# Kernel tuning notes

Measured on AMD Instinct MI355X. Metric: run time of the kernel, lower is better.

Reference implementation:

```python
import jax, jax.numpy as jnp
from jax import lax
import numpy as np

B, N, NPOINTS, DOWN_NUM, K = 4, 4096, 4096, 1024, 16
EPS = 1e-5


def setup_inputs() -> dict:
    key = jax.random.key(0)
    ks = jax.random.split(key, 8)
    w = lambda k, s: jax.random.normal(k, s, jnp.float32) * 0.05
    return {
        "x": jax.random.normal(ks[0], (B, 3, N), jnp.float32),
        "w_in": w(ks[1], (8, 3)), "b_in": jnp.zeros((8,), jnp.float32),
        "w1": w(ks[2], (32, 16)), "g1w": jnp.ones((32,), jnp.float32), "g1b": jnp.zeros((32,), jnp.float32),
        "w2": w(ks[3], (64, 64)), "g2w": jnp.ones((64,), jnp.float32), "g2b": jnp.zeros((64,), jnp.float32),
        "w3": w(ks[4], (64, 128)), "g3w": jnp.ones((64,), jnp.float32), "g3b": jnp.zeros((64,), jnp.float32),
        "w4": w(ks[5], (128, 128)), "g4w": jnp.ones((128,), jnp.float32), "g4b": jnp.zeros((128,), jnp.float32),
    }


def _knn_idx(coor_k, coor_q, k):
    # coor_*: (B,3,N) -> idx (B,Nq,k) of k nearest points in coor_k for each query
    q = coor_q.transpose(0, 2, 1)  # (B,Nq,3)
    r = coor_k.transpose(0, 2, 1)  # (B,Nk,3)
    d = (jnp.sum(q * q, -1)[:, :, None] + jnp.sum(r * r, -1)[:, None, :]
         - 2.0 * jnp.einsum('bqc,bkc->bqk', q, r))
    _, idx = lax.top_k(-d, k)  # smallest distances
    return idx


def _graph_feature(coor_q, x_q, coor_k, x_k, k):
    # gather k-NN neighbor features and concat (neighbor - center, center)
    idx = _knn_idx(coor_k, coor_q, k)           # (B,Nq,k)
    xk = x_k.transpose(0, 2, 1)                  # (B,Nk,C)
    b, nq, _ = idx.shape
    c = xk.shape[-1]
    feat = jnp.take_along_axis(xk, idx.reshape(b, nq * k)[..., None], axis=1)
    feat = feat.reshape(b, nq, k, c).transpose(0, 3, 1, 2)  # (B,C,Nq,k)
    xq = x_q[:, :, :, None]                      # (B,C,Nq,1)
    return jnp.concatenate([feat - xq, jnp.broadcast_to(xq, feat.shape)], axis=1)


def _fps_idx(xyz, m):
    # furthest point sampling, xyz (B,N,3) -> idx (B,m); starts at point 0
    b, n, _ = xyz.shape
    def body(carry, _):
        dists, farthest = carry
        centroid = jnp.take_along_axis(xyz, farthest[:, None, None], axis=1)  # (B,1,3)
        d = jnp.sum((xyz - centroid) ** 2, axis=-1)
        dists = jnp.minimum(dists, d)
        return (dists, jnp.argmax(dists, axis=-1)), farthest
    init = (jnp.full((b, n), 1e10, xyz.dtype), jnp.zeros((b,), jnp.int32))
    _, idx = lax.scan(body, init, None, length=m)
    return idx.T  # (B,m)


def _fps_downsample(coor, f, m):
    idx = _fps_idx(coor.transpose(0, 2, 1), m)        # (B,m)
    combined = jnp.concatenate([coor, f], axis=1)      # (B,3+C,N)
    new = jnp.take_along_axis(combined, idx[:, None, :], axis=2)
    return new[:, :3], new[:, 3:]


def _group_norm(x, w, b, groups=4):
    bsz, c = x.shape[0], x.shape[1]
    xr = x.reshape(bsz, groups, -1)
    m = xr.mean(-1, keepdims=True)
    v = xr.var(-1, keepdims=True)
    xn = ((xr - m) * lax.rsqrt(v + EPS)).reshape(x.shape)
    shp = (1, c) + (1,) * (x.ndim - 2)
    return xn * w.reshape(shp) + b.reshape(shp)


def _block(f, w, gw, gb):
    # 1x1 conv (no bias) -> GroupNorm(4) -> LeakyReLU(0.2) -> max over neighbors
    h = jnp.einsum('oc,bcnk->bonk', w, f)
    h = jax.nn.leaky_relu(_group_norm(h, gw, gb), negative_slope=0.2)
    return h.max(axis=-1)


def reference(x, w_in, b_in, w1, g1w, g1b, w2, g2w, g2b, w3, g3w, g3b, w4, g4w, g4b):
    coor = x
    f = jnp.einsum('oc,bcn->bon', w_in, x) + b_in[None, :, None]
    inpc_f = f
    f = _graph_feature(coor, f, coor, f, K)
    f = _block(f, w1, g1w, g1b)                      # (B,32,N)
    coor_q, f_q = _fps_downsample(coor, f, NPOINTS // 2)
    f = _graph_feature(coor_q, f_q, coor, f, K)
    f = _block(f, w2, g2w, g2b)                      # (B,64,N/2)
    xyz1, point1 = coor_q, f
    coor = coor_q
    f = _graph_feature(coor, f, coor, f, K)
    f = _block(f, w3, g3w, g3b)                      # (B,64,N/2)
    coor_q, f_q = _fps_downsample(coor, f, DOWN_NUM)
    f = _graph_feature(coor_q, f_q, coor, f, K)
    f = _block(f, w4, g4w, g4b)                      # (B,128,DOWN_NUM)
    coor = coor_q
    return (coor, f, xyz1, point1, inpc_f)
```

## Files before the change

kernel.cpp:

```cpp
#include <hip/hip_runtime.h>
#include <float.h>
#include <math.h>

static constexpr int BATCH = 4;
static constexpr int NPT0  = 4096;

static constexpr size_t OFF_F0T  = 0;
static constexpr size_t OFF_F1T  = 524288;
static constexpr size_t OFF_F2T  = 3670016;
static constexpr size_t OFF_F3T  = 5767168;
static constexpr size_t OFF_CQ1  = 8912896;
static constexpr size_t OFF_CQ2  = 9011200;
static constexpr size_t OFF_H    = 9060352;
static constexpr size_t OFF_IDX1 = 42614784;
static constexpr size_t OFF_IDX2 = 43663360;
static constexpr size_t OFF_IDX3 = 44187648;
static constexpr size_t OFF_IDX4 = 44711936;
static constexpr size_t OFF_FPS1 = 44974080;
static constexpr size_t OFF_FPS2 = 45006848;
static constexpr size_t OFF_WD1  = 45023232;
static constexpr size_t OFF_WD2  = 45024256;
static constexpr size_t OFF_WD3  = 45032448;
static constexpr size_t OFF_WD4  = 45048832;
static constexpr size_t OFF_STAT = 45081600;
static constexpr size_t OFF_PART  = 45099008;
static constexpr size_t OFF_PART2 = OFF_PART;
static constexpr size_t OFF_PART3 = OFF_PART + 8388608;
static constexpr size_t OFF_PART4 = OFF_PART + 12582912;

static constexpr size_t OUT_COOR = 0;
static constexpr size_t OUT_F    = 12288;
static constexpr size_t OUT_XYZ1 = 536576;
static constexpr size_t OUT_PT1  = 561152;
static constexpr size_t OUT_INPC = 1085440;

__device__ __forceinline__ void prep_dev(
    int vb, const float* __restrict__ w1, const float* __restrict__ w2,
    const float* __restrict__ w3, const float* __restrict__ w4,
    float* __restrict__ wd1, float* __restrict__ wd2,
    float* __restrict__ wd3, float* __restrict__ wd4,
    double* __restrict__ stats)
{
  int t = vb * 256 + threadIdx.x;
  if (t < 128) stats[t] = 0.0;
  if (t < 32 * 8)   { int o = t / 8,  c = t % 8;  wd1[t] = w1[o*16  + 8   + c] - w1[o*16  + c]; }
  if (t < 64 * 32)  { int o = t / 32, c = t % 32; wd2[t] = w2[o*64  + 32  + c] - w2[o*64  + c]; }
  if (t < 64 * 64)  { int o = t / 64, c = t % 64; wd3[t] = w3[o*128 + 64  + c] - w3[o*128 + c]; }
  if (t < 128 * 64) { int o = t / 64, c = t % 64; wd4[t] = w4[o*128 + 64  + c] - w4[o*128 + c]; }
}

__device__ __forceinline__ void linear_dev(
    int vb, const float* __restrict__ x, const float* __restrict__ w_in,
    const float* __restrict__ b_in, float* __restrict__ f0t,
    float* __restrict__ out_inpc)
{
  int t = vb * 256 + threadIdx.x;
  int n = t & (NPT0 - 1);
  int b = t >> 12;
  float x0 = x[(size_t)b*3*NPT0 + n];
  float x1 = x[(size_t)b*3*NPT0 + NPT0 + n];
  float x2 = x[(size_t)b*3*NPT0 + 2*NPT0 + n];
#pragma unroll
  for (int o = 0; o < 8; ++o) {
    float v = __fmul_rn(w_in[o*3], x0);
    v = fmaf(w_in[o*3+1], x1, v);
    v = fmaf(w_in[o*3+2], x2, v);
    v = __fadd_rn(v, b_in[o]);
    f0t[(size_t)t * 8 + o] = v;
    out_inpc[((size_t)b*8 + o)*NPT0 + n] = v;
  }
}

__device__ __forceinline__ void knnp_dev(
    int vb, const float* __restrict__ cq, const float* __restrict__ ck,
    unsigned long long* __restrict__ part, int Nq, int Nk, int slices, void* smem)
{
  const int CS = 512;
  int s  = vb % slices;
  int r  = vb / slices;
  int qb = r % (Nq >> 8);
  int b  = r / (Nq >> 8);
  float4* cand = (float4*)smem;
  int t = threadIdx.x;
  const float* ckb = ck + (size_t)b*3*Nk;
  for (int jj = t; jj < CS; jj += 256) {
    int j = s*CS + jj;
    float xx = ckb[j], yy = ckb[Nk + j], zz = ckb[2*Nk + j];
    float sq = __fadd_rn(__fadd_rn(__fmul_rn(xx,xx), __fmul_rn(yy,yy)), __fmul_rn(zz,zz));
    cand[jj] = make_float4(xx, yy, zz, sq);
  }
  __syncthreads();
  int q = qb*256 + t;
  const float* cqb = cq + (size_t)b*3*Nq;
  float qx = cqb[q], qy = cqb[Nq + q], qz = cqb[2*Nq + q];
  float sqq = __fadd_rn(__fadd_rn(__fmul_rn(qx,qx), __fmul_rn(qy,qy)), __fmul_rn(qz,qz));

  unsigned long long bd[16];
#pragma unroll
  for (int sl = 0; sl < 16; ++sl) bd[sl] = ~0ull;
  unsigned long long wk = ~0ull; int ws = 0;

  for (int jj = 0; jj < CS; ++jj) {
    float4 c = cand[jj];
    float dot = __fmul_rn(c.x, qx);
    dot = fmaf(c.y, qy, dot);
    dot = fmaf(c.z, qz, dot);
    float d = __fsub_rn(__fadd_rn(sqq, c.w), __fmul_rn(2.0f, dot));
    unsigned u = __float_as_uint(d);
    u ^= (0x80000000u | (unsigned)((int)u >> 31));
    unsigned long long key = ((unsigned long long)u << 32) | (unsigned)(s*CS + jj);
    if (key < wk) {
      unsigned long long nw = 0; int nws = 0;
#pragma unroll
      for (int sl = 0; sl < 16; ++sl) {
        bool rep = (sl == ws);
        unsigned long long v = rep ? key : bd[sl];
        bd[sl] = v;
        bool g = v > nw;
        nw = g ? v : nw; nws = g ? sl : nws;
      }
      wk = nw; ws = nws;
    }
  }
  unsigned long long* op = part + (((size_t)b*Nq + q)*(size_t)slices + s)*16;
#pragma unroll
  for (int sl = 0; sl < 16; ++sl) op[sl] = bd[sl];
}

__device__ __forceinline__ void merge_dev(
    int vb, const unsigned long long* __restrict__ part, int* __restrict__ idx,
    int slices)
{
  int t = vb * 256 + threadIdx.x;
  const unsigned long long* ip = part + (size_t)t * slices * 16;
  unsigned long long bd[16];
#pragma unroll
  for (int sl = 0; sl < 16; ++sl) bd[sl] = ~0ull;
  unsigned long long wk = ~0ull; int ws = 0;
  int n = slices * 16;
  for (int i = 0; i < n; ++i) {
    unsigned long long key = ip[i];
    if (key < wk) {
      unsigned long long nw = 0; int nws = 0;
#pragma unroll
      for (int sl = 0; sl < 16; ++sl) {
        bool rep = (sl == ws);
        unsigned long long v = rep ? key : bd[sl];
        bd[sl] = v;
        bool g = v > nw;
        nw = g ? v : nw; nws = g ? sl : nws;
      }
      wk = nw; ws = nws;
    }
  }
  int* op = idx + (size_t)t * 16;
#pragma unroll
  for (int sl = 0; sl < 16; ++sl) op[sl] = (int)(bd[sl] & 0xFFFFFFFFull);
}

__global__ __launch_bounds__(256) void k_merge(
    const unsigned long long* __restrict__ part, int* __restrict__ idx, int slices)
{
  merge_dev(blockIdx.x, part, idx, slices);
}

template<int NN, int PPT>
__device__ __forceinline__ void fps_dev(
    int b, const float* __restrict__ coor, int m, int* __restrict__ fidx_all,
    float* __restrict__ ca_all, float* __restrict__ co_all, void* smem)
{
  __builtin_amdgcn_s_setprio(3);
  float* sx = (float*)smem;
  float* sy = sx + NN;
  float* sz = sy + NN;
  unsigned long long* part = (unsigned long long*)(sz + NN);
  int t = threadIdx.x, lane = t & 63, wv = t >> 6;
  const float* cb = coor + (size_t)b*3*NN;
  float px[PPT], py[PPT], pz[PPT], pd[PPT];
  unsigned invj[PPT];
#pragma unroll
  for (int i = 0; i < PPT; ++i) {
    int j = i*256 + t;
    px[i] = cb[j]; py[i] = cb[NN + j]; pz[i] = cb[2*NN + j];
    pd[i] = 1e10f;
    invj[i] = (unsigned)(~j);
    sx[j] = px[i]; sy[j] = py[i]; sz[j] = pz[i];
  }
  __syncthreads();
  float cx = sx[0], cy = sy[0], cz = sz[0];
  int* fidx = fidx_all + b*m;
  float* ca = ca_all + (size_t)b*3*m;
  float* co = co_all + (size_t)b*3*m;
  int cur = 0, par = 0;
  for (int it = 0; it < m; ++it) {
    if (t == 0) {
      fidx[it] = cur;
      ca[it] = cx; ca[m + it] = cy; ca[2*m + it] = cz;
      co[it] = cx; co[m + it] = cy; co[2*m + it] = cz;
    }
    unsigned long long kk[PPT];
#pragma unroll
    for (int i = 0; i < PPT; ++i) {
      float dx = __fsub_rn(px[i], cx);
      float dy = __fsub_rn(py[i], cy);
      float dz = __fsub_rn(pz[i], cz);
      float d = __fadd_rn(__fadd_rn(__fmul_rn(dx,dx), __fmul_rn(dy,dy)), __fmul_rn(dz,dz));
      float nd = fminf(pd[i], d);
      pd[i] = nd;
      kk[i] = ((unsigned long long)__float_as_uint(nd) << 32) | invj[i];
    }
#pragma unroll
    for (int st = PPT/2; st >= 1; st >>= 1)
#pragma unroll
      for (int i = 0; i < st; ++i)
        if (kk[i + st] > kk[i]) kk[i] = kk[i + st];
    unsigned long long bk = kk[0];
#pragma unroll
    for (int mm = 1; mm < 64; mm <<= 1) {
      unsigned long long o = __shfl_xor(bk, mm, 64);
      bk = o > bk ? o : bk;
    }
    if (lane == 0) part[par*4 + wv] = bk;
    __syncthreads();
    ulonglong2 p01 = *(ulonglong2*)&part[par*4 + 0];
    ulonglong2 p23 = *(ulonglong2*)&part[par*4 + 2];
    unsigned long long k0 = p01.x > p01.y ? p01.x : p01.y;
    unsigned long long k2 = p23.x > p23.y ? p23.x : p23.y;
    k0 = k2 > k0 ? k2 : k0;
    cur = (int)(~(unsigned)(k0 & 0xFFFFFFFFull));
    cx = sx[cur]; cy = sy[cur]; cz = sz[cur];
    par ^= 1;
  }
}

template<int C, int COUT, int OC>
__device__ __forceinline__ void passA_dev(
    int vb, const float* __restrict__ xq, const float* __restrict__ xk,
    const int* __restrict__ idx, const float* __restrict__ w,
    const float* __restrict__ wdl, float* __restrict__ h,
    double* __restrict__ stats, int Nq, int Nk,
    const int* __restrict__ qmap, int NqSrc, void* smem)
{
  constexpr int NCH = COUT / OC;
  constexpr int GS  = COUT / 4;
  float* sxq   = (float*)smem;
  float* sbase = sxq + 16*C;
  int qb = Nq >> 4;
  int b = vb / qb, nb = vb % qb;
  int n0 = nb << 4;
  int t = threadIdx.x;
  for (int i = t; i < 16*C; i += 256) {
    int nn = i / C, cc = i % C;
    int qrow = qmap ? qmap[b*Nq + n0 + nn] : (n0 + nn);
    sxq[nn*C + cc] = xq[((size_t)b*NqSrc + qrow)*C + cc];
  }
  __syncthreads();
  for (int i = t; i < 16*COUT; i += 256) {
    int nn = i / COUT, o = i % COUT;
    float acc = 0.f;
#pragma unroll 4
    for (int c = 0; c < C; ++c) acc = fmaf(wdl[o*C + c], sxq[nn*C + c], acc);
    sbase[nn*(COUT+1) + o] = acc;
  }
  __syncthreads();
  int lane = t & 63;
  int n_loc = t >> 4, kk = t & 15;
  int kidx = idx[((size_t)b*Nq + n0 + n_loc)*16 + kk];
  const float* xr = xk + ((size_t)b*Nk + kidx)*C;
  float* hrow = h + (((size_t)b*Nq + n0 + n_loc)*16 + kk)*(size_t)COUT;
#pragma unroll 1
  for (int oc = 0; oc < NCH; ++oc) {
    int o0 = oc * OC;
    float acc[OC];
#pragma unroll
    for (int oi = 0; oi < OC; ++oi) acc[oi] = sbase[n_loc*(COUT+1) + o0 + oi];
#pragma unroll 1
    for (int c4 = 0; c4 < C/4; ++c4) {
      float4 v = *(const float4*)(xr + c4*4);
#pragma unroll
      for (int oi = 0; oi < OC; ++oi) {
        const float* wr = w + (size_t)(o0 + oi)*(2*C) + c4*4;
        acc[oi] = fmaf(wr[0], v.x, acc[oi]);
        acc[oi] = fmaf(wr[1], v.y, acc[oi]);
        acc[oi] = fmaf(wr[2], v.z, acc[oi]);
        acc[oi] = fmaf(wr[3], v.w, acc[oi]);
      }
    }
#pragma unroll
    for (int oi = 0; oi < OC; ++oi) hrow[o0 + oi] = acc[oi];
    double s = 0.0, s2 = 0.0;
#pragma unroll
    for (int oi = 0; oi < OC; ++oi) { double dv = (double)acc[oi]; s += dv; s2 += dv*dv; }
#pragma unroll
    for (int mm = 1; mm < 64; mm <<= 1) {
      s  += __shfl_xor(s,  mm, 64);
      s2 += __shfl_xor(s2, mm, 64);
    }
    if (lane == 0) {
      int g = o0 / GS;
      atomicAdd(&stats[((size_t)b*4 + g)*2],     s);
      atomicAdd(&stats[((size_t)b*4 + g)*2 + 1], s2);
    }
  }
}

template<int C, int COUT, int OC>
__global__ __launch_bounds__(256) void k_passA(
    const float* __restrict__ xq, const float* __restrict__ xk,
    const int* __restrict__ idx, const float* __restrict__ w,
    const float* __restrict__ wdl, float* __restrict__ h,
    double* __restrict__ stats, int Nq, int Nk,
    const int* __restrict__ qmap, int NqSrc)
{
  extern __shared__ char smem[];
  passA_dev<C,COUT,OC>(blockIdx.x, xq, xk, idx, w, wdl, h, stats, Nq, Nk,
                       qmap, NqSrc, smem);
}

__device__ __forceinline__ void passB_dev(
    int vb, const float* __restrict__ h, const double* __restrict__ stats,
    const float* __restrict__ gw, const float* __restrict__ gb,
    float* __restrict__ ft, float* __restrict__ ocn, int Nq, int COUT)
{
  int t = vb * 256 + threadIdx.x;
  int o = t % COUT;
  int r = t / COUT;
  int n = r % Nq;
  int b = r / Nq;
  int GS = COUT / 4, g = o / GS;
  double cnt = (double)GS * (double)Nq * 16.0;
  double su = stats[((size_t)b*4 + g)*2];
  double s2 = stats[((size_t)b*4 + g)*2 + 1];
  double mean = su / cnt;
  double var = s2 / cnt - mean * mean;
  float vf = (float)var; if (vf < 0.f) vf = 0.f;
  float inv = 1.0f / sqrtf(vf + 1e-5f);
  float A = gw[o] * inv;
  float Bb = gb[o] - (float)mean * A;
  const float* hp = h + (((size_t)b*Nq + n)*16)*(size_t)COUT + o;
  float m = -FLT_MAX;
#pragma unroll
  for (int k = 0; k < 16; ++k) {
    float v = hp[(size_t)k*COUT];
    float y = fmaf(v, A, Bb);
    y = (y >= 0.f) ? y : 0.2f*y;
    m = fmaxf(m, y);
  }
  if (ft)  ft[((size_t)b*Nq + n)*COUT + o] = m;
  if (ocn) ocn[((size_t)b*COUT + o)*Nq + n] = m;
}

__global__ __launch_bounds__(256) void k_passB(
    const float* __restrict__ h, const double* __restrict__ stats,
    const float* __restrict__ gw, const float* __restrict__ gb,
    float* __restrict__ ft, float* __restrict__ ocn, int Nq, int COUT)
{
  passB_dev(blockIdx.x, h, stats, gw, gb, ft, ocn, Nq, COUT);
}

__global__ __launch_bounds__(256) void k_megaA(
    const float* __restrict__ x, const float* __restrict__ w_in,
    const float* __restrict__ b_in, float* __restrict__ f0t,
    float* __restrict__ outInpc,
    const float* __restrict__ w1, const float* __restrict__ w2,
    const float* __restrict__ w3, const float* __restrict__ w4,
    float* __restrict__ wd1, float* __restrict__ wd2,
    float* __restrict__ wd3, float* __restrict__ wd4,
    double* __restrict__ stats,
    int* __restrict__ fps1, float* __restrict__ cq1, float* __restrict__ outXyz1,
    unsigned long long* __restrict__ part1)
{
  extern __shared__ char smem[];
  int vb = blockIdx.x;
  if      (vb < 4)   fps_dev<4096,16>(vb, x, 2048, fps1, cq1, outXyz1, smem);
  else if (vb < 36)  prep_dev(vb - 4, w1, w2, w3, w4, wd1, wd2, wd3, wd4, stats);
  else if (vb < 100) linear_dev(vb - 36, x, w_in, b_in, f0t, outInpc);
  else               knnp_dev(vb - 100, x, x, part1, 4096, 4096, 8, smem);
}

__global__ __launch_bounds__(256) void k_megaB(
    const float* __restrict__ cq1, const float* __restrict__ x,
    int* __restrict__ fps2, float* __restrict__ cq2, float* __restrict__ outCoor,
    unsigned long long* __restrict__ part2, unsigned long long* __restrict__ part3,
    const float* __restrict__ f0t, const int* __restrict__ idx1,
    const float* __restrict__ w1, const float* __restrict__ wd1,
    float* __restrict__ h, double* __restrict__ st1)
{
  extern __shared__ char smem[];
  int vb = blockIdx.x;
  if      (vb < 4)           fps_dev<2048,8>(vb, cq1, 1024, fps2, cq2, outCoor, smem);
  else if (vb < 4 + 256)     knnp_dev(vb - 4,   cq1, x,   part2, 2048, 4096, 8, smem);
  else if (vb < 4 + 256+128) knnp_dev(vb - 260, cq1, cq1, part3, 2048, 2048, 4, smem);
  else                       passA_dev<8,32,8>(vb - 388, f0t, f0t, idx1, w1, wd1,
                                               h, st1, 4096, 4096, nullptr, 4096, smem);
}

__global__ __launch_bounds__(256) void k_megaC(
    const float* __restrict__ cq2, const float* __restrict__ cq1,
    unsigned long long* __restrict__ part4,
    const unsigned long long* __restrict__ part2, int* __restrict__ idx2,
    const unsigned long long* __restrict__ part3, int* __restrict__ idx3,
    const float* __restrict__ h, const double* __restrict__ st1,
    const float* __restrict__ g1w, const float* __restrict__ g1b,
    float* __restrict__ f1t)
{
  extern __shared__ char smem[];
  int vb = blockIdx.x;
  if      (vb < 64)  knnp_dev(vb, cq2, cq1, part4, 1024, 2048, 4, smem);
  else if (vb < 96)  merge_dev(vb - 64, part2, idx2, 8);
  else if (vb < 128) merge_dev(vb - 96, part3, idx3, 4);
  else               passB_dev(vb - 128, h, st1, g1w, g1b, f1t, nullptr, 4096, 32);
}

__global__ __launch_bounds__(256) void k_megaD(
    const unsigned long long* __restrict__ part4, int* __restrict__ idx4,
    const float* __restrict__ f1t, const int* __restrict__ idx2,
    const float* __restrict__ w2, const float* __restrict__ wd2,
    float* __restrict__ h, double* __restrict__ st2,
    const int* __restrict__ fps1)
{
  extern __shared__ char smem[];
  int vb = blockIdx.x;
  if (vb < 16) merge_dev(vb, part4, idx4, 4);
  else         passA_dev<32,64,16>(vb - 16, f1t, f1t, idx2, w2, wd2, h, st2,
                                   2048, 4096, fps1, 4096, smem);
}

extern "C" void kernel_launch(void* const* d_in, const int* in_sizes, int n_in,
                              void* d_out, int out_size, void* d_ws, size_t ws_size,
                              hipStream_t stream)
{
  (void)in_sizes; (void)n_in; (void)out_size; (void)ws_size;
  const float* x    = (const float*)d_in[0];
  const float* w_in = (const float*)d_in[1];
  const float* b_in = (const float*)d_in[2];
  const float* w1   = (const float*)d_in[3];
  const float* g1w  = (const float*)d_in[4];
  const float* g1b  = (const float*)d_in[5];
  const float* w2   = (const float*)d_in[6];
  const float* g2w  = (const float*)d_in[7];
  const float* g2b  = (const float*)d_in[8];
  const float* w3   = (const float*)d_in[9];
  const float* g3w  = (const float*)d_in[10];
  const float* g3b  = (const float*)d_in[11];
  const float* w4   = (const float*)d_in[12];
  const float* g4w  = (const float*)d_in[13];
  const float* g4b  = (const float*)d_in[14];
  float* out = (float*)d_out;
  char*  wsb = (char*)d_ws;

  float* f0t  = (float*)(wsb + OFF_F0T);
  float* f1t  = (float*)(wsb + OFF_F1T);
  float* f2t  = (float*)(wsb + OFF_F2T);
  float* f3t  = (float*)(wsb + OFF_F3T);
  float* cq1  = (float*)(wsb + OFF_CQ1);
  float* cq2  = (float*)(wsb + OFF_CQ2);
  float* h    = (float*)(wsb + OFF_H);
  int*   idx1 = (int*)(wsb + OFF_IDX1);
  int*   idx2 = (int*)(wsb + OFF_IDX2);
  int*   idx3 = (int*)(wsb + OFF_IDX3);
  int*   idx4 = (int*)(wsb + OFF_IDX4);
  int*   fps1 = (int*)(wsb + OFF_FPS1);
  int*   fps2 = (int*)(wsb + OFF_FPS2);
  float* wd1  = (float*)(wsb + OFF_WD1);
  float* wd2  = (float*)(wsb + OFF_WD2);
  float* wd3  = (float*)(wsb + OFF_WD3);
  float* wd4  = (float*)(wsb + OFF_WD4);
  double* statAll = (double*)(wsb + OFF_STAT);
  double* st1 = statAll, *st2 = statAll + 32, *st3 = statAll + 64, *st4 = statAll + 96;
  unsigned long long* part1 = (unsigned long long*)(wsb + OFF_PART);
  unsigned long long* part2 = (unsigned long long*)(wsb + OFF_PART2);
  unsigned long long* part3 = (unsigned long long*)(wsb + OFF_PART3);
  unsigned long long* part4 = (unsigned long long*)(wsb + OFF_PART4);

  float* outCoor = out + OUT_COOR;
  float* outF    = out + OUT_F;
  float* outXyz1 = out + OUT_XYZ1;
  float* outPt1  = out + OUT_PT1;
  float* outInpc = out + OUT_INPC;

  k_megaA<<<612, 256, 49216, stream>>>(x, w_in, b_in, f0t, outInpc,
      w1, w2, w3, w4, wd1, wd2, wd3, wd4, statAll, fps1, cq1, outXyz1, part1);
  k_merge<<<64, 256, 0, stream>>>(part1, idx1, 8);

  k_megaB<<<1412, 256, 24640, stream>>>(
      cq1, x, fps2, cq2, outCoor, part2, part3, f0t, idx1, w1, wd1, h, st1);

  k_megaC<<<2176, 256, 8192, stream>>>(
      cq2, cq1, part4, part2, idx2, part3, idx3, h, st1, g1w, g1b, f1t);

  k_megaD<<<528, 256, 6208, stream>>>(part4, idx4, f1t, idx2, w2, wd2, h, st2, fps1);

  k_passB<<<2048, 256, 0, stream>>>(h, st2, g2w, g2b, f2t, outPt1, 2048, 64);
  k_passA<64,64,16><<<512, 256, 8256, stream>>>(f2t, f2t, idx3, w3, wd3, h, st3,
                                                2048, 2048, nullptr, 2048);
  k_passB<<<2048, 256, 0, stream>>>(h, st3, g3w, g3b, f3t, nullptr, 2048, 64);
  k_passA<64,128,16><<<256, 256, 12352, stream>>>(f3t, f3t, idx4, w4, wd4, h, st4,
                                                  1024, 2048, fps2, 2048);
  k_passB<<<2048, 256, 0, stream>>>(h, st4, g4w, g4b, nullptr, outF, 1024, 128);
}
```

Measured before the change: 3.397 ms.

## Precompute packed candidate arrays, widen KNN slices, and use DPP reductions in FPS

Adds a pre-kernel that packs candidate coordinates plus squared norms into float4 arrays in global memory. KNN partial blocks now stream these packed candidates directly instead of staging them in LDS, with 1024-wide slices, which halves the slice count and the work in the later merges. The FPS loop replaces the 64-bit key tree and shuffle reduction with a float argmax followed by a DPP row reduction, and drops the priority boost. Kernels are re-split so FPS shares its launch with fewer co-resident blocks; this adds one extra launch and relies on KNN blocks overlapping the serial FPS.

```diff
diff --git a/kernel.cpp b/kernel.cpp
--- a/kernel.cpp
+++ b/kernel.cpp
@@ -25,14 +25,25 @@
 static constexpr size_t OFF_STAT = 45081600;
 static constexpr size_t OFF_PART  = 45099008;
 static constexpr size_t OFF_PART2 = OFF_PART;
-static constexpr size_t OFF_PART3 = OFF_PART + 8388608;
-static constexpr size_t OFF_PART4 = OFF_PART + 12582912;
+static constexpr size_t OFF_PART3 = OFF_PART + 4194304;
+static constexpr size_t OFF_PART4 = OFF_PART + 6291456;
+static constexpr size_t OFF_CAND0 = 53487616;
+static constexpr size_t OFF_CAND1 = 53749760;
 
 static constexpr size_t OUT_COOR = 0;
 static constexpr size_t OUT_F    = 12288;
 static constexpr size_t OUT_XYZ1 = 536576;
 static constexpr size_t OUT_PT1  = 561152;
 static constexpr size_t OUT_INPC = 1085440;
+
+template<int CTRL>
+__device__ __forceinline__ unsigned long long dpp_max64(unsigned long long k) {
+  unsigned lo = (unsigned)k, hi = (unsigned)(k >> 32);
+  unsigned olo = (unsigned)__builtin_amdgcn_update_dpp((int)lo, (int)lo, CTRL, 0xF, 0xF, false);
+  unsigned ohi = (unsigned)__builtin_amdgcn_update_dpp((int)hi, (int)hi, CTRL, 0xF, 0xF, false);
+  unsigned long long o = ((unsigned long long)ohi << 32) | olo;
+  return o > k ? o : k;
+}
 
 __device__ __forceinline__ void prep_dev(
     int vb, const float* __restrict__ w1, const float* __restrict__ w2,
@@ -71,7 +82,59 @@
   }
 }
 
-__device__ __forceinline__ void knnp_dev(
+template<int CS>
+__device__ __forceinline__ void knnp_pack_dev(
+    int vb, const float* __restrict__ cq, const float4* __restrict__ candPack,
+    unsigned long long* __restrict__ part, int Nq, int Nk)
+{
+  const int slices = Nk / CS;
+  int s  = vb % slices;
+  int r  = vb / slices;
+  int qb = r % (Nq >> 8);
+  int b  = r / (Nq >> 8);
+  int t  = threadIdx.x;
+  int q  = qb*256 + t;
+  const float* cqb = cq + (size_t)b*3*Nq;
+  float qx = cqb[q], qy = cqb[Nq + q], qz = cqb[2*Nq + q];
+  float sqq = __fadd_rn(__fadd_rn(__fmul_rn(qx,qx), __fmul_rn(qy,qy)), __fmul_rn(qz,qz));
+
+  const float4* cp = candPack + (size_t)b*Nk + s*CS;
+  int jbase = s*CS;
+
+  unsigned long long bd[16];
+#pragma unroll
+  for (int sl = 0; sl < 16; ++sl) bd[sl] = ~0ull;
+  unsigned long long wk = ~0ull; int ws = 0;
+
+#pragma unroll 4
+  for (int jj = 0; jj < CS; ++jj) {
+    float4 c = cp[jj];
+    float dot = __fmul_rn(c.x, qx);
+    dot = fmaf(c.y, qy, dot);
+    dot = fmaf(c.z, qz, dot);
+    float d = __fsub_rn(__fadd_rn(sqq, c.w), __fmul_rn(2.0f, dot));
+    unsigned u = __float_as_uint(d);
+    u ^= (0x80000000u | (unsigned)((int)u >> 31));
+    unsigned long long key = ((unsigned long long)u << 32) | (unsigned)(jbase + jj);
+    if (key < wk) {
+      unsigned long long nw = 0; int nws = 0;
+#pragma unroll
+      for (int sl = 0; sl < 16; ++sl) {
+        bool rep = (sl == ws);
+        unsigned long long v = rep ? key : bd[sl];
+        bd[sl] = v;
+        bool g = v > nw;
+        nw = g ? v : nw; nws = g ? sl : nws;
+      }
+      wk = nw; ws = nws;
+    }
+  }
+  unsigned long long* op = part + (((size_t)b*Nq + q)*(size_t)slices + s)*16;
+#pragma unroll
+  for (int sl = 0; sl < 16; ++sl) op[sl] = bd[sl];
+}
+
+__device__ __forceinline__ void knnp_lds_dev(
     int vb, const float* __restrict__ cq, const float* __restrict__ ck,
     unsigned long long* __restrict__ part, int Nq, int Nk, int slices, void* smem)
 {
@@ -158,18 +221,11 @@
   for (int sl = 0; sl < 16; ++sl) op[sl] = (int)(bd[sl] & 0xFFFFFFFFull);
 }
 
-__global__ __launch_bounds__(256) void k_merge(
-    const unsigned long long* __restrict__ part, int* __restrict__ idx, int slices)
-{
-  merge_dev(blockIdx.x, part, idx, slices);
-}
-
 template<int NN, int PPT>
 __device__ __forceinline__ void fps_dev(
     int b, const float* __restrict__ coor, int m, int* __restrict__ fidx_all,
     float* __restrict__ ca_all, float* __restrict__ co_all, void* smem)
 {
-  __builtin_amdgcn_s_setprio(3);
   float* sx = (float*)smem;
   float* sy = sx + NN;
   float* sz = sy + NN;
@@ -177,13 +233,11 @@
   int t = threadIdx.x, lane = t & 63, wv = t >> 6;
   const float* cb = coor + (size_t)b*3*NN;
   float px[PPT], py[PPT], pz[PPT], pd[PPT];
-  unsigned invj[PPT];
 #pragma unroll
   for (int i = 0; i < PPT; ++i) {
     int j = i*256 + t;
     px[i] = cb[j]; py[i] = cb[NN + j]; pz[i] = cb[2*NN + j];
     pd[i] = 1e10f;
-    invj[i] = (unsigned)(~j);
     sx[j] = px[i]; sy[j] = py[i]; sz[j] = pz[i];
   }
   __syncthreads();
@@ -198,7 +252,7 @@
       ca[it] = cx; ca[m + it] = cy; ca[2*m + it] = cz;
       co[it] = cx; co[m + it] = cy; co[2*m + it] = cz;
     }
-    unsigned long long kk[PPT];
+    float bv = -1.0f; int bslot = 0;
 #pragma unroll
     for (int i = 0; i < PPT; ++i) {
       float dx = __fsub_rn(px[i], cx);
@@ -207,25 +261,26 @@
       float d = __fadd_rn(__fadd_rn(__fmul_rn(dx,dx), __fmul_rn(dy,dy)), __fmul_rn(dz,dz));
       float nd = fminf(pd[i], d);
       pd[i] = nd;
-      kk[i] = ((unsigned long long)__float_as_uint(nd) << 32) | invj[i];
-    }
-#pragma unroll
-    for (int st = PPT/2; st >= 1; st >>= 1)
-#pragma unroll
-      for (int i = 0; i < st; ++i)
-        if (kk[i + st] > kk[i]) kk[i] = kk[i + st];
-    unsigned long long bk = kk[0];
-#pragma unroll
-    for (int mm = 1; mm < 64; mm <<= 1) {
-      unsigned long long o = __shfl_xor(bk, mm, 64);
-      bk = o > bk ? o : bk;
-    }
-    if (lane == 0) part[par*4 + wv] = bk;
+      bool g = nd > bv;
+      bv = g ? nd : bv;
+      bslot = g ? i : bslot;
+    }
+    unsigned bij = ~(unsigned)((bslot << 8) | t);
+    unsigned long long k = ((unsigned long long)__float_as_uint(bv) << 32) | bij;
+    k = dpp_max64<0x111>(k);
+    k = dpp_max64<0x112>(k);
+    k = dpp_max64<0x114>(k);
+    k = dpp_max64<0x118>(k);
+    k = dpp_max64<0x142>(k);
+    k = dpp_max64<0x143>(k);
+    unsigned wlo = (unsigned)__builtin_amdgcn_readlane((int)(unsigned)k, 63);
+    unsigned whi = (unsigned)__builtin_amdgcn_readlane((int)(unsigned)(k >> 32), 63);
+    if (lane == 0) part[par*4 + wv] = ((unsigned long long)whi << 32) | wlo;
     __syncthreads();
-    ulonglong2 p01 = *(ulonglong2*)&part[par*4 + 0];
-    ulonglong2 p23 = *(ulonglong2*)&part[par*4 + 2];
-    unsigned long long k0 = p01.x > p01.y ? p01.x : p01.y;
-    unsigned long long k2 = p23.x > p23.y ? p23.x : p23.y;
+    unsigned long long k0 = part[par*4 + 0], k1 = part[par*4 + 1];
+    unsigned long long k2 = part[par*4 + 2], k3 = part[par*4 + 3];
+    k0 = k1 > k0 ? k1 : k0;
+    k2 = k3 > k2 ? k3 : k2;
     k0 = k2 > k0 ? k2 : k0;
     cur = (int)(~(unsigned)(k0 & 0xFFFFFFFFull));
     cx = sx[cur]; cy = sy[cur]; cz = sz[cur];
@@ -358,7 +413,7 @@
   passB_dev(blockIdx.x, h, stats, gw, gb, ft, ocn, Nq, COUT);
 }
 
-__global__ __launch_bounds__(256) void k_megaA(
+__global__ __launch_bounds__(256) void k_pre(
     const float* __restrict__ x, const float* __restrict__ w_in,
     const float* __restrict__ b_in, float* __restrict__ f0t,
     float* __restrict__ outInpc,
@@ -366,20 +421,51 @@
     const float* __restrict__ w3, const float* __restrict__ w4,
     float* __restrict__ wd1, float* __restrict__ wd2,
     float* __restrict__ wd3, float* __restrict__ wd4,
-    double* __restrict__ stats,
-    int* __restrict__ fps1, float* __restrict__ cq1, float* __restrict__ outXyz1,
-    unsigned long long* __restrict__ part1)
+    double* __restrict__ stats, float4* __restrict__ cand0)
+{
+  int vb = blockIdx.x;
+  if (vb < 64) {
+    int g = vb*256 + threadIdx.x;
+    int b = g >> 12, n = g & 4095;
+    const float* xb = x + (size_t)b*3*4096;
+    float xx = xb[n], yy = xb[4096 + n], zz = xb[2*4096 + n];
+    float sq = __fadd_rn(__fadd_rn(__fmul_rn(xx,xx), __fmul_rn(yy,yy)), __fmul_rn(zz,zz));
+    cand0[g] = make_float4(xx, yy, zz, sq);
+  }
+  else if (vb < 96) prep_dev(vb - 64, w1, w2, w3, w4, wd1, wd2, wd3, wd4, stats);
+  else              linear_dev(vb - 96, x, w_in, b_in, f0t, outInpc);
+}
+
+__global__ __launch_bounds__(256, 2) void k_megaA(
+    const float* __restrict__ x, int* __restrict__ fps1,
+    float* __restrict__ cq1, float* __restrict__ outXyz1,
+    const float4* __restrict__ cand0, unsigned long long* __restrict__ part1)
 {
   extern __shared__ char smem[];
   int vb = blockIdx.x;
-  if      (vb < 4)   fps_dev<4096,16>(vb, x, 2048, fps1, cq1, outXyz1, smem);
-  else if (vb < 36)  prep_dev(vb - 4, w1, w2, w3, w4, wd1, wd2, wd3, wd4, stats);
-  else if (vb < 100) linear_dev(vb - 36, x, w_in, b_in, f0t, outInpc);
-  else               knnp_dev(vb - 100, x, x, part1, 4096, 4096, 8, smem);
-}
-
-__global__ __launch_bounds__(256) void k_megaB(
-    const float* __restrict__ cq1, const float* __restrict__ x,
+  if (vb < 4) fps_dev<4096,16>(vb, x, 2048, fps1, cq1, outXyz1, smem);
+  else        knnp_pack_dev<1024>(vb - 4, x, cand0, part1, 4096, 4096);
+}
+
+__global__ __launch_bounds__(256) void k_mergeP(
+    const unsigned long long* __restrict__ part1, int* __restrict__ idx1,
+    const float* __restrict__ cq1, float4* __restrict__ cand1)
+{
+  int vb = blockIdx.x;
+  if (vb < 64) merge_dev(vb, part1, idx1, 4);
+  else {
+    int g = (vb - 64)*256 + threadIdx.x;
+    int b = g >> 11, n = g & 2047;
+    const float* cb = cq1 + (size_t)b*3*2048;
+    float xx = cb[n], yy = cb[2048 + n], zz = cb[2*2048 + n];
+    float sq = __fadd_rn(__fadd_rn(__fmul_rn(xx,xx), __fmul_rn(yy,yy)), __fmul_rn(zz,zz));
+    cand1[g] = make_float4(xx, yy, zz, sq);
+  }
+}
+
+__global__ __launch_bounds__(256, 2) void k_megaB(
+    const float* __restrict__ cq1, const float4* __restrict__ cand0,
+    const float4* __restrict__ cand1,
     int* __restrict__ fps2, float* __restrict__ cq2, float* __restrict__ outCoor,
     unsigned long long* __restrict__ part2, unsigned long long* __restrict__ part3,
     const float* __restrict__ f0t, const int* __restrict__ idx1,
@@ -388,11 +474,11 @@
 {
   extern __shared__ char smem[];
   int vb = blockIdx.x;
-  if      (vb < 4)           fps_dev<2048,8>(vb, cq1, 1024, fps2, cq2, outCoor, smem);
-  else if (vb < 4 + 256)     knnp_dev(vb - 4,   cq1, x,   part2, 2048, 4096, 8, smem);
-  else if (vb < 4 + 256+128) knnp_dev(vb - 260, cq1, cq1, part3, 2048, 2048, 4, smem);
-  else                       passA_dev<8,32,8>(vb - 388, f0t, f0t, idx1, w1, wd1,
-                                               h, st1, 4096, 4096, nullptr, 4096, smem);
+  if      (vb < 4)          fps_dev<2048,8>(vb, cq1, 1024, fps2, cq2, outCoor, smem);
+  else if (vb < 4 + 128)    knnp_pack_dev<1024>(vb - 4,   cq1, cand0, part2, 2048, 4096);
+  else if (vb < 4 + 128+64) knnp_pack_dev<1024>(vb - 132, cq1, cand1, part3, 2048, 2048);
+  else                      passA_dev<8,32,8>(vb - 196, f0t, f0t, idx1, w1, wd1,
+                                              h, st1, 4096, 4096, nullptr, 4096, smem);
 }
 
 __global__ __launch_bounds__(256) void k_megaC(
@@ -406,9 +492,9 @@
 {
   extern __shared__ char smem[];
   int vb = blockIdx.x;
-  if      (vb < 64)  knnp_dev(vb, cq2, cq1, part4, 1024, 2048, 4, smem);
-  else if (vb < 96)  merge_dev(vb - 64, part2, idx2, 8);
-  else if (vb < 128) merge_dev(vb - 96, part3, idx3, 4);
+  if      (vb < 64)  knnp_lds_dev(vb, cq2, cq1, part4, 1024, 2048, 4, smem);
+  else if (vb < 96)  merge_dev(vb - 64, part2, idx2, 4);
+  else if (vb < 128) merge_dev(vb - 96, part3, idx3, 2);
   else               passB_dev(vb - 128, h, st1, g1w, g1b, f1t, nullptr, 4096, 32);
 }
 
@@ -472,6 +558,8 @@
   unsigned long long* part2 = (unsigned long long*)(wsb + OFF_PART2);
   unsigned long long* part3 = (unsigned long long*)(wsb + OFF_PART3);
   unsigned long long* part4 = (unsigned long long*)(wsb + OFF_PART4);
+  float4* cand0 = (float4*)(wsb + OFF_CAND0);
+  float4* cand1 = (float4*)(wsb + OFF_CAND1);
 
   float* outCoor = out + OUT_COOR;
   float* outF    = out + OUT_F;
@@ -479,12 +567,15 @@
   float* outPt1  = out + OUT_PT1;
   float* outInpc = out + OUT_INPC;
 
-  k_megaA<<<612, 256, 49216, stream>>>(x, w_in, b_in, f0t, outInpc,
-      w1, w2, w3, w4, wd1, wd2, wd3, wd4, statAll, fps1, cq1, outXyz1, part1);
-  k_merge<<<64, 256, 0, stream>>>(part1, idx1, 8);
-
-  k_megaB<<<1412, 256, 24640, stream>>>(
-      cq1, x, fps2, cq2, outCoor, part2, part3, f0t, idx1, w1, wd1, h, st1);
+  k_pre<<<160, 256, 0, stream>>>(x, w_in, b_in, f0t, outInpc,
+      w1, w2, w3, w4, wd1, wd2, wd3, wd4, statAll, cand0);
+
+  k_megaA<<<260, 256, 49216, stream>>>(x, fps1, cq1, outXyz1, cand0, part1);
+
+  k_mergeP<<<96, 256, 0, stream>>>(part1, idx1, cq1, cand1);
+
+  k_megaB<<<1220, 256, 24640, stream>>>(
+      cq1, cand0, cand1, fps2, cq2, outCoor, part2, part3, f0t, idx1, w1, wd1, h, st1);
 
   k_megaC<<<2176, 256, 8192, stream>>>(
       cq2, cq1, part4, part2, idx2, part3, idx3, h, st1, g1w, g1b, f1t);
```

Measured after the change: 3.037 ms. 1.12x faster.
